# Kernel tuning notes

Hardware: AMD Instinct MI355X
Metric: run time of the kernel (lower is better)

Reference implementation:

```python
import math
import jax, jax.numpy as jnp
import numpy as np

B, S, D, H = 4, 1024, 512, 8
DH = D // H  # 64
SQRT_DIM = math.sqrt(D)


def _relative_shift(pos_score):
    # pos_score: [B, H, S, S]
    b, h, s1, s2 = pos_score.shape
    zeros = jnp.zeros((b, h, s1, 1), dtype=pos_score.dtype)
    padded = jnp.concatenate([zeros, pos_score], axis=-1)      # [B,H,S,S+1]
    padded = padded.reshape(b, h, s2 + 1, s1)                  # [B,H,S+1,S]
    return padded[:, :, 1:].reshape(b, h, s1, s2)


def setup_inputs() -> dict:
    key = jax.random.key(0)
    ks = jax.random.split(key, 14)
    std = 0.02
    inp = {
        "query": jax.random.normal(ks[0], (B, S, D), jnp.float32),
        "key": jax.random.normal(ks[1], (B, S, D), jnp.float32),
        "value": jax.random.normal(ks[2], (B, S, D), jnp.float32),
        "pos_embedding": jax.random.normal(ks[3], (B, S, D), jnp.float32),
        # projection weights stored [in, out] so y = x @ W + b
        "Wq": jax.random.normal(ks[4], (D, D), jnp.float32) * std,
        "bq": jnp.zeros((D,), jnp.float32),
        "Wk": jax.random.normal(ks[5], (D, D), jnp.float32) * std,
        "bk": jnp.zeros((D,), jnp.float32),
        "Wv": jax.random.normal(ks[6], (D, D), jnp.float32) * std,
        "bv": jnp.zeros((D,), jnp.float32),
        "Wp": jax.random.normal(ks[7], (D, D), jnp.float32) * std,  # pos_proj, no bias
        "Wo": jax.random.normal(ks[8], (D, D), jnp.float32) * std,
        "bo": jnp.zeros((D,), jnp.float32),
        "u_bias": jax.random.normal(ks[9], (H, DH), jnp.float32) * std,
        "v_bias": jax.random.normal(ks[10], (H, DH), jnp.float32) * std,
    }
    return inp


def reference(query, key, value, pos_embedding, Wq, bq, Wk, bk, Wv, bv, Wp, Wo, bo, u_bias, v_bias):
    b = query.shape[0]
    q = (query @ Wq + bq).reshape(b, -1, H, DH)          # [B,S,H,DH]
    k = (key @ Wk + bk).reshape(b, -1, H, DH)            # [B,T,H,DH]
    v = (value @ Wv + bv).reshape(b, -1, H, DH)          # [B,T,H,DH]
    p = (pos_embedding @ Wp).reshape(b, -1, H, DH)       # [B,T,H,DH]

    # content score: (q + u) . k  -> [B,H,S,T]
    content_score = jnp.einsum('bshd,bthd->bhst', q + u_bias, k)
    # position score: (q + v) . pos -> [B,H,S,T], then relative shift
    pos_score = jnp.einsum('bshd,bthd->bhst', q + v_bias, p)
    pos_score = _relative_shift(pos_score)

    score = (content_score + pos_score) / SQRT_DIM
    attn = jax.nn.softmax(score, axis=-1)                # dropout p=0 (eval)

    context = jnp.einsum('bhst,bthd->bshd', attn, v).reshape(b, -1, D)
    out = context @ Wo + bo
    return (out, attn)
```

## Files before the change

### kernel.cpp

```cpp
#include <hip/hip_runtime.h>

#define B_  4
#define S_  1024
#define D_  512
#define H_  8
#define DH_ 64
#define SCALE 0.044194173824159216f

typedef short bf16x8 __attribute__((ext_vector_type(8)));
typedef float f32x4  __attribute__((ext_vector_type(4)));

__device__ __forceinline__ unsigned short f2bf(float x) {
    union { float f; unsigned int u; } v; v.f = x;
    unsigned int r = v.u + 0x7fffu + ((v.u >> 16) & 1u);
    return (unsigned short)(r >> 16);
}
__device__ __forceinline__ float bf2f(unsigned short h) {
    union { unsigned int u; float f; } v; v.u = ((unsigned int)h) << 16;
    return v.f;
}

__global__ __launch_bounds__(256) void convert_wt_k(
    const float* __restrict__ W0, const float* __restrict__ W1,
    const float* __restrict__ W2, const float* __restrict__ W3,
    const float* __restrict__ W4,
    unsigned short* __restrict__ T0, unsigned short* __restrict__ T1,
    unsigned short* __restrict__ T2, unsigned short* __restrict__ T3,
    unsigned short* __restrict__ T4)
{
    __shared__ float tile[64][65];
    const float* W;
    unsigned short* T;
    switch (blockIdx.z) {
        case 0: W = W0; T = T0; break;
        case 1: W = W1; T = T1; break;
        case 2: W = W2; T = T2; break;
        case 3: W = W3; T = T3; break;
        default: W = W4; T = T4; break;
    }
    const int r0 = blockIdx.y * 64, c0 = blockIdx.x * 64;
    const int tx = threadIdx.x & 63, ty = threadIdx.x >> 6;
#pragma unroll
    for (int it = 0; it < 16; ++it)
        tile[ty + 4 * it][tx] = W[(size_t)(r0 + ty + 4 * it) * 512 + c0 + tx];
    __syncthreads();
#pragma unroll
    for (int it = 0; it < 16; ++it)
        T[(size_t)(c0 + ty + 4 * it) * 512 + r0 + tx] = f2bf(tile[tx][ty + 4 * it]);
}

__global__ __launch_bounds__(512) void proj_all_k(
    const float* __restrict__ Aq_, const float* __restrict__ Ak_,
    const float* __restrict__ Ap_, const float* __restrict__ Av_,
    const unsigned short* __restrict__ WqT, const unsigned short* __restrict__ WkT,
    const unsigned short* __restrict__ WpT, const unsigned short* __restrict__ WvT,
    const float* __restrict__ bq, const float* __restrict__ bk,
    const float* __restrict__ bv,
    const float* __restrict__ ub, const float* __restrict__ vb,
    unsigned short* __restrict__ qu, unsigned short* __restrict__ qv,
    unsigned short* __restrict__ kbf, unsigned short* __restrict__ pbf,
    unsigned short* __restrict__ v2)
{
    __shared__ unsigned short Ab[128][72];
    __shared__ unsigned short Bb[128][72];
    const int mode = blockIdx.z;
    const float* A;
    const unsigned short* BT;
    switch (mode) {
        case 0: A = Aq_; BT = WqT; break;
        case 1: A = Ak_; BT = WkT; break;
        case 2: A = Ap_; BT = WpT; break;
        default: A = Av_; BT = WvT; break;
    }
    const int tid = threadIdx.x;
    const int i0 = blockIdx.x * 128, j0 = blockIdx.y * 128;
    const int w = tid >> 6, lane = tid & 63, l15 = lane & 15, lhi = lane >> 4;
    const int mr0 = (w >> 1) * 32, nc0 = (w & 1) * 64;
    f32x4 acc[2][4] = {};

    for (int k0 = 0; k0 < 512; k0 += 64) {
        __syncthreads();
#pragma unroll
        for (int it = 0; it < 4; ++it) {
            const int s = tid + it * 512;
            const int row = s >> 4, f4 = (s & 15) * 4;
            float4 va = *(const float4*)&A[(size_t)(i0 + row) * 512 + k0 + f4];
            ushort4 hh;
            hh.x = f2bf(va.x); hh.y = f2bf(va.y); hh.z = f2bf(va.z); hh.w = f2bf(va.w);
            *(ushort4*)&Ab[row][f4] = hh;
        }
#pragma unroll
        for (int it = 0; it < 2; ++it) {
            const int s = tid + it * 512;
            const int row = s >> 3, g = (s & 7) * 8;
            *(bf16x8*)&Bb[row][g] = *(const bf16x8*)&BT[(size_t)(j0 + row) * 512 + k0 + g];
        }
        __syncthreads();
#pragma unroll
        for (int kk = 0; kk < 2; ++kk) {
            bf16x8 a0 = *(const bf16x8*)&Ab[mr0 + l15][kk * 32 + lhi * 8];
            bf16x8 a1 = *(const bf16x8*)&Ab[mr0 + 16 + l15][kk * 32 + lhi * 8];
#pragma unroll
            for (int n = 0; n < 4; ++n) {
                bf16x8 bn = *(const bf16x8*)&Bb[nc0 + 16 * n + l15][kk * 32 + lhi * 8];
                acc[0][n] = __builtin_amdgcn_mfma_f32_16x16x32_bf16(a0, bn, acc[0][n], 0, 0, 0);
                acc[1][n] = __builtin_amdgcn_mfma_f32_16x16x32_bf16(a1, bn, acc[1][n], 0, 0, 0);
            }
        }
    }

#pragma unroll
    for (int m = 0; m < 2; ++m)
#pragma unroll
        for (int n = 0; n < 4; ++n)
#pragma unroll
            for (int r = 0; r < 4; ++r) {
                const int grow = i0 + mr0 + 16 * m + 4 * lhi + r;
                const int gcol = j0 + nc0 + 16 * n + l15;
                const int b = grow >> 10, s = grow & 1023;
                const int h = gcol >> 6, d = gcol & 63;
                const float v = acc[m][n][r];
                if (mode == 3) {
                    const size_t idx = (((size_t)(b * H_ + h) * 32 + (s >> 5)) * 64 + d) * 32 + (s & 31);
                    v2[idx] = f2bf(v + bv[gcol]);
                } else {
                    const size_t idx = (((size_t)b * H_ + h) * S_ + s) * DH_ + d;
                    if (mode == 0) {
                        const float base = v + bq[gcol];
                        qu[idx] = f2bf(base + ub[gcol]);
                        qv[idx] = f2bf(base + vb[gcol]);
                    } else if (mode == 1) {
                        kbf[idx] = f2bf(v + bk[gcol]);
                    } else {
                        pbf[idx] = f2bf(v);
                    }
                }
            }
}

__global__ __launch_bounds__(256) void gemm_bf16_k(
    const unsigned short* __restrict__ A,
    const unsigned short* __restrict__ BT,
    const float* __restrict__ bias,
    float* __restrict__ C)
{
    __shared__ unsigned short Ab[64][72];
    __shared__ unsigned short Bb[64][72];
    const int tid = threadIdx.x;
    const int i0 = blockIdx.x * 64, j0 = blockIdx.y * 64;
    const int w = tid >> 6, lane = tid & 63, l15 = lane & 15, lhi = lane >> 4;
    const int mr0 = (w >> 1) * 32, nc0 = (w & 1) * 32;
    f32x4 acc[2][2] = {};

    for (int k0 = 0; k0 < 512; k0 += 64) {
        __syncthreads();
#pragma unroll
        for (int it = 0; it < 2; ++it) {
            const int s = tid + it * 256;
            const int row = s >> 3, g = (s & 7) * 8;
            *(bf16x8*)&Ab[row][g] = *(const bf16x8*)&A[(size_t)(i0 + row) * 512 + k0 + g];
            *(bf16x8*)&Bb[row][g] = *(const bf16x8*)&BT[(size_t)(j0 + row) * 512 + k0 + g];
        }
        __syncthreads();
#pragma unroll
        for (int kk = 0; kk < 2; ++kk) {
            bf16x8 a0 = *(const bf16x8*)&Ab[mr0 + l15][kk * 32 + lhi * 8];
            bf16x8 a1 = *(const bf16x8*)&Ab[mr0 + 16 + l15][kk * 32 + lhi * 8];
            bf16x8 b0 = *(const bf16x8*)&Bb[nc0 + l15][kk * 32 + lhi * 8];
            bf16x8 b1 = *(const bf16x8*)&Bb[nc0 + 16 + l15][kk * 32 + lhi * 8];
            acc[0][0] = __builtin_amdgcn_mfma_f32_16x16x32_bf16(a0, b0, acc[0][0], 0, 0, 0);
            acc[0][1] = __builtin_amdgcn_mfma_f32_16x16x32_bf16(a0, b1, acc[0][1], 0, 0, 0);
            acc[1][0] = __builtin_amdgcn_mfma_f32_16x16x32_bf16(a1, b0, acc[1][0], 0, 0, 0);
            acc[1][1] = __builtin_amdgcn_mfma_f32_16x16x32_bf16(a1, b1, acc[1][1], 0, 0, 0);
        }
    }

#pragma unroll
    for (int m = 0; m < 2; ++m)
#pragma unroll
        for (int n = 0; n < 2; ++n)
#pragma unroll
            for (int r = 0; r < 4; ++r) {
                const int grow = i0 + mr0 + 16 * m + 4 * lhi + r;
                const int gcol = j0 + nc0 + 16 * n + l15;
                C[(size_t)grow * 512 + gcol] = acc[m][n][r] + bias[gcol];
            }
}

#define RS 1032
#define QBLK 16

__global__ __launch_bounds__(512, 4) void score_fused_k(
    const unsigned short* __restrict__ qu_g,
    const unsigned short* __restrict__ qv_g,
    const unsigned short* __restrict__ kb_g,
    const unsigned short* __restrict__ pb_g,
    const unsigned short* __restrict__ v2_g,
    float* __restrict__ attn,
    unsigned short* __restrict__ ctx_g)
{
    __shared__ unsigned short Kb[128][72];
    __shared__ unsigned short Pb[128][72];
    __shared__ unsigned short Rsh[16 * RS];
    __shared__ float red[16][9];

    const int tid = threadIdx.x;
    const int i0 = blockIdx.x * QBLK;
    const int bh = blockIdx.y;
    const int w = tid >> 6, lane = tid & 63, l15 = lane & 15, lhi = lane >> 4;

    const unsigned short* qu_b = qu_g + (size_t)bh * S_ * DH_;
    const unsigned short* qv_b = qv_g + (size_t)bh * S_ * DH_;
    const unsigned short* kb_b = kb_g + (size_t)bh * S_ * DH_;
    const unsigned short* pb_b = pb_g + (size_t)bh * S_ * DH_;

    if (tid < 16) {
        const int j = i0 + tid + 1;
        if (j <= 1023) Rsh[tid * RS + j] = 0;
    }

    bf16x8 qf[2], aq0[2], aq1[2];
    {
        const int qrow  = i0 + l15;
        const int qrow1 = min(i0 + 16 + l15, S_ - 1);
#pragma unroll
        for (int kk = 0; kk < 2; ++kk) {
            const int off = kk * 32 + lhi * 8;
            qf[kk]  = *(const bf16x8*)&qu_b[(size_t)qrow  * DH_ + off];
            aq0[kk] = *(const bf16x8*)&qv_b[(size_t)qrow  * DH_ + off];
            aq1[kk] = *(const bf16x8*)&qv_b[(size_t)qrow1 * DH_ + off];
        }
    }

    const int srow0 = 16 * w + (lane >> 3);
    const int sseg  = (lane & 7) * 8;

    bf16x8 kreg[2], preg[2];
#pragma unroll
    for (int it = 0; it < 2; ++it) {
        const size_t g = (size_t)(srow0 + it * 8) * DH_ + sseg;
        kreg[it] = *(const bf16x8*)&kb_b[g];
        preg[it] = *(const bf16x8*)&pb_b[g];
    }

    f32x4 acc[8] = {};
#pragma unroll
    for (int jc = 0; jc < 8; ++jc) {
#pragma unroll
        for (int it = 0; it < 2; ++it) {
            *(bf16x8*)&Kb[srow0 + it * 8][sseg] = kreg[it];
            *(bf16x8*)&Pb[srow0 + it * 8][sseg] = preg[it];
        }
        if (jc < 7) {
#pragma unroll
            for (int it = 0; it < 2; ++it) {
                const size_t g = (size_t)((jc + 1) * 128 + srow0 + it * 8) * DH_ + sseg;
                kreg[it] = *(const bf16x8*)&kb_b[g];
                preg[it] = *(const bf16x8*)&pb_b[g];
            }
        }

        f32x4 racc0 = {}, racc1 = {};
#pragma unroll
        for (int kk = 0; kk < 2; ++kk) {
            bf16x8 pfr = *(const bf16x8*)&Pb[16 * w + l15][kk * 32 + lhi * 8];
            bf16x8 kfr = *(const bf16x8*)&Kb[16 * w + l15][kk * 32 + lhi * 8];
            racc0 = __builtin_amdgcn_mfma_f32_16x16x32_bf16(aq0[kk], pfr, racc0, 0, 0, 0);
            racc1 = __builtin_amdgcn_mfma_f32_16x16x32_bf16(aq1[kk], pfr, racc1, 0, 0, 0);
            acc[jc] = __builtin_amdgcn_mfma_f32_16x16x32_bf16(qf[kk], kfr, acc[jc], 0, 0, 0);
        }

        const int u = jc * 128 + 16 * w + l15;
#pragma unroll
        for (int r = 0; r < 4; ++r) {
            const int rl = 4 * lhi + r;
            const int gr = i0 + rl;
            const int jlo = u + gr - 1023;
            const unsigned short val = f2bf(racc0[r]);
            if (jlo >= 0)      Rsh[rl * RS + jlo] = val;
            else if (rl >= 1)  Rsh[(rl - 1) * RS + (u + gr + 1)] = val;
        }
        if (lhi == 0) {
            const int jhi = u + i0 + 17;
            if (jhi <= 1023) Rsh[15 * RS + jhi] = f2bf(racc1[0]);
        }
    }
    __syncthreads();

    const int il = 4 * lhi;
    float rmax[4], rsum[4];
#pragma unroll
    for (int r = 0; r < 4; ++r) rmax[r] = -3.0e38f;

#pragma unroll
    for (int jc = 0; jc < 8; ++jc)
#pragma unroll
        for (int r = 0; r < 4; ++r) {
            const int row = il + r;
            const int j = jc * 128 + 16 * w + l15;
            const float pos = bf2f(Rsh[row * RS + j]);
            const float s = (acc[jc][r] + pos) * SCALE;
            acc[jc][r] = s;
            rmax[r] = fmaxf(rmax[r], s);
        }

#pragma unroll
    for (int r = 0; r < 4; ++r)
#pragma unroll
        for (int off = 1; off < 16; off <<= 1)
            rmax[r] = fmaxf(rmax[r], __shfl_xor(rmax[r], off));
    if (l15 == 0)
#pragma unroll
        for (int r = 0; r < 4; ++r) red[il + r][w] = rmax[r];
    __syncthreads();
#pragma unroll
    for (int r = 0; r < 4; ++r) {
        float mx = red[il + r][0];
#pragma unroll
        for (int ww = 1; ww < 8; ++ww) mx = fmaxf(mx, red[il + r][ww]);
        rmax[r] = mx;
        rsum[r] = 0.f;
    }
    __syncthreads();

#pragma unroll
    for (int jc = 0; jc < 8; ++jc)
#pragma unroll
        for (int r = 0; r < 4; ++r) {
            const float e = __expf(acc[jc][r] - rmax[r]);
            acc[jc][r] = e;
            rsum[r] += e;
        }
#pragma unroll
    for (int r = 0; r < 4; ++r)
#pragma unroll
        for (int off = 1; off < 16; off <<= 1)
            rsum[r] += __shfl_xor(rsum[r], off);
    if (l15 == 0)
#pragma unroll
        for (int r = 0; r < 4; ++r) red[il + r][w] = rsum[r];
    __syncthreads();

    float* attn_b = attn + (size_t)bh * S_ * S_;
#pragma unroll
    for (int r = 0; r < 4; ++r) {
        float sum = red[il + r][0];
#pragma unroll
        for (int ww = 1; ww < 8; ++ww) sum += red[il + r][ww];
        const float inv = 1.f / sum;
#pragma unroll
        for (int jc = 0; jc < 8; ++jc) {
            const int j = jc * 128 + 16 * w + l15;
            const float pn = acc[jc][r] * inv;
            attn_b[(size_t)(i0 + il + r) * S_ + j] = pn;
            Rsh[(il + r) * RS + j] = f2bf(pn);
        }
    }
    __syncthreads();

    const int b4 = bh >> 3, h4 = bh & 7;
    const int nblk = w & 3;
    const int kh = w >> 2;
    const unsigned short* v2b = v2_g + (size_t)bh * 32 * 2048;
    const int dd = 16 * nblk + l15;
    f32x4 cacc = {};
#pragma unroll
    for (int half = 0; half < 2; ++half) {
        bf16x8 bbuf[8];
#pragma unroll
        for (int ki = 0; ki < 8; ++ki) {
            const int tb = kh * 16 + half * 8 + ki;
            bbuf[ki] = *(const bf16x8*)&v2b[(size_t)tb * 2048 + dd * 32 + lhi * 8];
        }
#pragma unroll
        for (int ki = 0; ki < 8; ++ki) {
            const int t0 = (kh * 16 + half * 8 + ki) * 32 + lhi * 8;
            bf16x8 a = *(const bf16x8*)&Rsh[l15 * RS + t0];
            cacc = __builtin_amdgcn_mfma_f32_16x16x32_bf16(a, bbuf[ki], cacc, 0, 0, 0);
        }
    }
    float* fred = (float*)&Kb[0][0];
    if (kh == 0) {
#pragma unroll
        for (int r = 0; r < 4; ++r)
            fred[(nblk * 16 + 4 * lhi + r) * 16 + l15] = cacc[r];
    }
    __syncthreads();
    if (kh == 1) {
#pragma unroll
        for (int r = 0; r < 4; ++r) {
            const float vs = cacc[r] + fred[(nblk * 16 + 4 * lhi + r) * 16 + l15];
            const int srow = i0 + 4 * lhi + r;
            ctx_g[((size_t)(b4 * S_ + srow)) * D_ + h4 * DH_ + 16 * nblk + l15] = f2bf(vs);
        }
    }
}

extern "C" void kernel_launch(void* const* d_in, const int* in_sizes, int n_in,
                              void* d_out, int out_size, void* d_ws, size_t ws_size,
                              hipStream_t stream)
{
    const float* query = (const float*)d_in[0];
    const float* key_  = (const float*)d_in[1];
    const float* value = (const float*)d_in[2];
    const float* pose  = (const float*)d_in[3];
    const float* Wq = (const float*)d_in[4];
    const float* bq = (const float*)d_in[5];
    const float* Wk = (const float*)d_in[6];
    const float* bk = (const float*)d_in[7];
    const float* Wv = (const float*)d_in[8];
    const float* bv = (const float*)d_in[9];
    const float* Wp = (const float*)d_in[10];
    const float* Wo = (const float*)d_in[11];
    const float* bo = (const float*)d_in[12];
    const float* u_bias = (const float*)d_in[13];
    const float* v_bias = (const float*)d_in[14];

    const size_t NTOK = (size_t)B_ * S_ * D_;
    float* out  = (float*)d_out;
    float* attn = (float*)d_out + NTOK;

    unsigned short* qu  = (unsigned short*)d_ws;
    unsigned short* qv  = qu + NTOK;
    unsigned short* kbf = qv + NTOK;
    unsigned short* pbf = kbf + NTOK;
    unsigned short* WqT = pbf + NTOK;
    unsigned short* WkT = WqT + 262144;
    unsigned short* WpT = WkT + 262144;
    unsigned short* WvT = WpT + 262144;
    unsigned short* WoT = WvT + 262144;
    unsigned short* v2  = WoT + 262144;
    unsigned short* ctx = v2 + NTOK;

    const dim3 blk256(256);
    const dim3 gproj(64, 8);

    convert_wt_k<<<dim3(8, 8, 5), blk256, 0, stream>>>(Wq, Wk, Wp, Wv, Wo,
                                                       WqT, WkT, WpT, WvT, WoT);

    proj_all_k<<<dim3(32, 4, 4), dim3(512), 0, stream>>>(
        query, key_, pose, value,
        WqT, WkT, WpT, WvT,
        bq, bk, bv, u_bias, v_bias,
        qu, qv, kbf, pbf, v2);

    score_fused_k<<<dim3(S_ / QBLK, B_ * H_), dim3(512), 0, stream>>>(
        qu, qv, kbf, pbf, v2, attn, ctx);

    gemm_bf16_k<<<gproj, blk256, 0, stream>>>(ctx, WoT, bo, out);
}
```

Before: 116.6 us.

## Share one LDS staging buffer for K and P tiles to raise occupancy

Replaces the separate K and P shared-memory tiles in the fused score kernel with a single buffer. Each chunk now stages the K tile, runs the content MFMAs, then overwrites the same buffer with the P tile for the positional MFMAs. This cuts LDS use per block so more blocks can be resident per CU, and the launch bound is raised from 4 to 6 to match. In exchange the K and P phases are serialized within each chunk, and the tighter launch bound may squeeze registers and cause spills.

```diff
diff --git a/kernel.cpp b/kernel.cpp
--- a/kernel.cpp
+++ b/kernel.cpp
@@ -190,7 +190,7 @@
 #define RS 1032
 #define QBLK 16
 
-__global__ __launch_bounds__(512, 4) void score_fused_k(
+__global__ __launch_bounds__(512, 6) void score_fused_k(
     const unsigned short* __restrict__ qu_g,
     const unsigned short* __restrict__ qv_g,
     const unsigned short* __restrict__ kb_g,
@@ -199,8 +199,7 @@
     float* __restrict__ attn,
     unsigned short* __restrict__ ctx_g)
 {
-    __shared__ unsigned short Kb[128][72];
-    __shared__ unsigned short Pb[128][72];
+    __shared__ unsigned short Sb[128][72];
     __shared__ unsigned short Rsh[16 * RS];
     __shared__ float red[16][9];
 
@@ -247,27 +246,39 @@
 #pragma unroll
     for (int jc = 0; jc < 8; ++jc) {
 #pragma unroll
-        for (int it = 0; it < 2; ++it) {
-            *(bf16x8*)&Kb[srow0 + it * 8][sseg] = kreg[it];
-            *(bf16x8*)&Pb[srow0 + it * 8][sseg] = preg[it];
-        }
+        for (int it = 0; it < 2; ++it)
+            *(bf16x8*)&Sb[srow0 + it * 8][sseg] = kreg[it];
         if (jc < 7) {
 #pragma unroll
             for (int it = 0; it < 2; ++it) {
                 const size_t g = (size_t)((jc + 1) * 128 + srow0 + it * 8) * DH_ + sseg;
                 kreg[it] = *(const bf16x8*)&kb_b[g];
+            }
+        }
+        {
+            bf16x8 kf0 = *(const bf16x8*)&Sb[16 * w + l15][lhi * 8];
+            bf16x8 kf1 = *(const bf16x8*)&Sb[16 * w + l15][32 + lhi * 8];
+            acc[jc] = __builtin_amdgcn_mfma_f32_16x16x32_bf16(qf[0], kf0, acc[jc], 0, 0, 0);
+            acc[jc] = __builtin_amdgcn_mfma_f32_16x16x32_bf16(qf[1], kf1, acc[jc], 0, 0, 0);
+        }
+#pragma unroll
+        for (int it = 0; it < 2; ++it)
+            *(bf16x8*)&Sb[srow0 + it * 8][sseg] = preg[it];
+        if (jc < 7) {
+#pragma unroll
+            for (int it = 0; it < 2; ++it) {
+                const size_t g = (size_t)((jc + 1) * 128 + srow0 + it * 8) * DH_ + sseg;
                 preg[it] = *(const bf16x8*)&pb_b[g];
             }
         }
-
         f32x4 racc0 = {}, racc1 = {};
-#pragma unroll
-        for (int kk = 0; kk < 2; ++kk) {
-            bf16x8 pfr = *(const bf16x8*)&Pb[16 * w + l15][kk * 32 + lhi * 8];
-            bf16x8 kfr = *(const bf16x8*)&Kb[16 * w + l15][kk * 32 + lhi * 8];
-            racc0 = __builtin_amdgcn_mfma_f32_16x16x32_bf16(aq0[kk], pfr, racc0, 0, 0, 0);
-            racc1 = __builtin_amdgcn_mfma_f32_16x16x32_bf16(aq1[kk], pfr, racc1, 0, 0, 0);
-            acc[jc] = __builtin_amdgcn_mfma_f32_16x16x32_bf16(qf[kk], kfr, acc[jc], 0, 0, 0);
+        {
+            bf16x8 pf0 = *(const bf16x8*)&Sb[16 * w + l15][lhi * 8];
+            bf16x8 pf1 = *(const bf16x8*)&Sb[16 * w + l15][32 + lhi * 8];
+            racc0 = __builtin_amdgcn_mfma_f32_16x16x32_bf16(aq0[0], pf0, racc0, 0, 0, 0);
+            racc0 = __builtin_amdgcn_mfma_f32_16x16x32_bf16(aq0[1], pf1, racc0, 0, 0, 0);
+            racc1 = __builtin_amdgcn_mfma_f32_16x16x32_bf16(aq1[0], pf0, racc1, 0, 0, 0);
+            racc1 = __builtin_amdgcn_mfma_f32_16x16x32_bf16(aq1[1], pf1, racc1, 0, 0, 0);
         }
 
         const int u = jc * 128 + 16 * w + l15;
@@ -379,7 +390,7 @@
             cacc = __builtin_amdgcn_mfma_f32_16x16x32_bf16(a, bbuf[ki], cacc, 0, 0, 0);
         }
     }
-    float* fred = (float*)&Kb[0][0];
+    float* fred = (float*)&Sb[0][0];
     if (kh == 0) {
 #pragma unroll
         for (int r = 0; r < 4; ++r)
```

Result: slower. 163.8 us (+40.5%).
